# Optimization experiments

Measured on AMD Instinct MI355X. Metric: run time of the kernel, lower is better.

## Reference

```python
import jax, jax.numpy as jnp
import numpy as np

# Scalar quantization params (QLinear __init__ args)
FEATURE_BITWIDTH = 8
WEIGHT_BITWIDTH = 8
INPUT_ZERO_POINT = -3
OUTPUT_ZERO_POINT = -5
INPUT_SCALE = 0.05
OUTPUT_SCALE = 0.1
QMIN = -(1 << (FEATURE_BITWIDTH - 1))   # -128
QMAX = (1 << (FEATURE_BITWIDTH - 1)) - 1  # 127

M, K, N = 8192, 4096, 4096


def float_to_fixed_point(x, bitwidth):
    """Represent x (0 < x < 1) as int_scale * 2^-frac_bits with int_scale
    in [2^(bitwidth-2), 2^(bitwidth-1)) (mantissa fits in signed `bitwidth` bits)."""
    frac_bits = (bitwidth - 1 - jnp.ceil(jnp.log2(x))).astype(jnp.int32)
    int_scale = jnp.round(x * jnp.exp2(frac_bits.astype(jnp.float32))).astype(jnp.int32)
    return int_scale, frac_bits


def setup_inputs() -> dict:
    key = jax.random.key(0)
    k1, k2, k3, k4 = jax.random.split(key, 4)
    qinput = jax.random.randint(k1, (M, K), -128, 128, dtype=jnp.int8)
    qweight = jax.random.randint(k2, (N, K), -128, 128, dtype=jnp.int8)
    qbias = jax.random.randint(k3, (N,), -(1 << 16), 1 << 16, dtype=jnp.int32)
    # per-output-channel weight scale; keeps folded scale in (0, 1)
    weight_scale = jax.random.uniform(k4, (N,), jnp.float32, 0.002, 0.02)
    return {"qinput": qinput, "qweight": qweight, "qbias": qbias,
            "weight_scale": weight_scale}


def reference(qinput, qweight, qbias, weight_scale):
    w32 = qweight.astype(jnp.int32)                      # [N, K]
    # Qbias' = qbias - sum_k(qweight) * Zin  (bias shift folding input zero point)
    shifted_qbias = qbias - w32.sum(axis=1) * INPUT_ZERO_POINT  # [N]
    # int32 GEMM: [M, K] @ [K, N] + bias
    acc = qinput.astype(jnp.int32) @ w32.T + shifted_qbias[None, :]  # [M, N]
    # fixed-point requantization: (acc * int_scale) >> frac_bits + Zout
    folded_scale = INPUT_SCALE * weight_scale / OUTPUT_SCALE         # [N], in (0,1)
    int_scale, frac_bits = float_to_fixed_point(folded_scale, FEATURE_BITWIDTH)
    # widen to int64 for the multiply so the (acc * int_scale) product cannot wrap
    prod = acc.astype(jnp.int64) * int_scale.astype(jnp.int64)[None, :]
    scaled = jnp.right_shift(prod, frac_bits.astype(jnp.int64)[None, :])  # arithmetic >>
    out = scaled + OUTPUT_ZERO_POINT
    return jnp.clip(out, QMIN, QMAX).astype(jnp.int8)
```

## Files before the change

kernel.cpp:

```cpp
#include <hip/hip_runtime.h>
#include <cstdint>
#include <cstddef>

#define M_DIM 8192
#define N_DIM 4096
#define K_DIM 4096

#define BM 128
#define BN 128
#define BK 128

#define BM2 256
#define BN2 256
#define BK2 128
#define NKT (K_DIM / BK2)

typedef int int32x4  __attribute__((ext_vector_type(4)));
typedef int int32x16 __attribute__((ext_vector_type(16)));


typedef __attribute__((address_space(1))) const void* gas_cptr;
typedef __attribute__((address_space(3))) void* las_ptr;

__device__ __forceinline__ void async_copy16(const void* g, void* l) {
    __builtin_amdgcn_global_load_lds((gas_cptr)g, (las_ptr)l, 16, 0, 0);
}

__device__ __forceinline__ int32x4 pack16(const int* p) {
    const int32x4* v = (const int32x4*)p;
    int32x4 w0 = v[0], w1 = v[1], w2 = v[2], w3 = v[3];
    int32x4 r;
    r.x = (w0.x & 0xFF) | ((w0.y & 0xFF) << 8) | ((w0.z & 0xFF) << 16) | (w0.w << 24);
    r.y = (w1.x & 0xFF) | ((w1.y & 0xFF) << 8) | ((w1.z & 0xFF) << 16) | (w1.w << 24);
    r.z = (w2.x & 0xFF) | ((w2.y & 0xFF) << 8) | ((w2.z & 0xFF) << 16) | (w2.w << 24);
    r.w = (w3.x & 0xFF) | ((w3.y & 0xFF) << 8) | ((w3.z & 0xFF) << 16) | (w3.w << 24);
    return r;
}

__global__ void ql_detect_kernel(const int* a, const int* b, int* ws) {
    int t = threadIdx.x;
    int fa = 0, fb = 0;
    for (int i = t; i < 4096; i += 64) {
        int va = a[i]; if (va > 127 || va < -128) fa = 1;
        int vb = b[i]; if (vb > 127 || vb < -128) fb = 1;
    }
    unsigned long long ba = __ballot(fa);
    unsigned long long bb = __ballot(fb);
    if (t == 0) { ws[0] = ba ? 1 : 0; ws[1] = bb ? 1 : 0; }
}

#define PACK_WBLK 4096
#define PACK_ABLK 8192
__global__ __launch_bounds__(256)
void ql_pack2_kernel(const void* wsrc, int* wdst, const void* asrc, int* adst,
                     const int* qbias, const float* wscale, int* ws) {
    __shared__ int red[4];
    const int fA = __builtin_amdgcn_readfirstlane(ws[0]);
    const int fW = __builtin_amdgcn_readfirstlane(ws[1]);
    const int bid = blockIdx.x;
    const int tid = threadIdx.x;
    if (bid < PACK_WBLK) {
        if (fW) return;
        const int n = bid;
        const int32x4* src = (const int32x4*)wsrc + (size_t)n * 1024;
        int* dst = wdst + (size_t)n * 1024;
        int s = 0;
#pragma unroll
        for (int k = 0; k < 4; ++k) {
            const int i = k * 256 + tid;
            int32x4 v = src[i];
            s += v.x + v.y + v.z + v.w;
            dst[i] = (v.x & 0xFF) | ((v.y & 0xFF) << 8) | ((v.z & 0xFF) << 16) | (v.w << 24);
        }
#pragma unroll
        for (int off = 32; off > 0; off >>= 1) s += __shfl_down(s, off, 64);
        if ((tid & 63) == 0) red[tid >> 6] = s;
        __syncthreads();
        if (tid == 0) {
            const int st = red[0] + red[1] + red[2] + red[3];
            ws[16 + n] = qbias[n] + 3 * st;
            float folded = (0.05f * wscale[n]) / 0.1f;
            int fbits = (int)(7.0f - ceilf(log2f(folded)));
            int isc = (int)rintf(folded * exp2f((float)fbits));
            ws[16 + N_DIM + n] = isc;
            ws[16 + 2 * N_DIM + n] = fbits;
        }
    } else {
        if (fA) return;
        const long base = (long)(bid - PACK_WBLK) * 1024;
        const int32x4* src = (const int32x4*)asrc + base;
        int* dst = adst + base;
#pragma unroll
        for (int k = 0; k < 4; ++k) {
            const int i = k * 256 + tid;
            int32x4 v = src[i];
            dst[i] = (v.x & 0xFF) | ((v.y & 0xFF) << 8) | ((v.z & 0xFF) << 16) | (v.w << 24);
        }
    }
}

__global__ void ql_prep8_kernel(const void* worig, const int* qbias,
                                const float* wscale, int* ws) {
    const int fb = __builtin_amdgcn_readfirstlane(ws[1]);
    if (!fb) return;

    const int lane = threadIdx.x & 63;
    const int wid  = threadIdx.x >> 6;
    const int n = blockIdx.x * 4 + wid;

    const int32x4* row = (const int32x4*)((const int8_t*)worig + (size_t)n * K_DIM);
    int s = 0;
    for (int c = lane; c < K_DIM / 16; c += 64) {
        int32x4 v = row[c];
#pragma unroll
        for (int j = 0; j < 4; ++j) {
            int w = (j == 0) ? v.x : (j == 1) ? v.y : (j == 2) ? v.z : v.w;
            s += (int)(int8_t)(w) + (int)(int8_t)(w >> 8)
               + (int)(int8_t)(w >> 16) + (w >> 24);
        }
    }
#pragma unroll
    for (int off = 32; off > 0; off >>= 1) s += __shfl_down(s, off, 64);

    if (lane == 0) {
        ws[16 + n] = qbias[n] + 3 * s;
        float folded = (0.05f * wscale[n]) / 0.1f;
        int fbits = (int)(7.0f - ceilf(log2f(folded)));
        int isc = (int)rintf(folded * exp2f((float)fbits));
        ws[16 + N_DIM + n] = isc;
        ws[16 + 2 * N_DIM + n] = fbits;
    }
}

__global__ void ql_prep_kernel(const void* wptr, const int* qbias,
                               const float* wscale, int* ws) {
    const int lane = threadIdx.x & 63;
    const int wid  = threadIdx.x >> 6;
    const int n = blockIdx.x * 4 + wid;
    const int b8 = __builtin_amdgcn_readfirstlane(ws[1]);

    int s = 0;
    if (b8) {
        const int32x4* row = (const int32x4*)((const int8_t*)wptr + (size_t)n * K_DIM);
        for (int c = lane; c < K_DIM / 16; c += 64) {
            int32x4 v = row[c];
#pragma unroll
            for (int j = 0; j < 4; ++j) {
                int w = (j == 0) ? v.x : (j == 1) ? v.y : (j == 2) ? v.z : v.w;
                s += (int)(int8_t)(w) + (int)(int8_t)(w >> 8)
                   + (int)(int8_t)(w >> 16) + (w >> 24);
            }
        }
    } else {
        const int32x4* row = (const int32x4*)((const int*)wptr + (size_t)n * K_DIM);
        for (int c = lane; c < K_DIM / 4; c += 64) {
            int32x4 v = row[c];
            s += v.x + v.y + v.z + v.w;
        }
    }
#pragma unroll
    for (int off = 32; off > 0; off >>= 1) s += __shfl_down(s, off, 64);

    if (lane == 0) {
        ws[16 + n] = qbias[n] + 3 * s;
        float folded = (0.05f * wscale[n]) / 0.1f;
        int fbits = (int)(7.0f - ceilf(log2f(folded)));
        int isc = (int)rintf(folded * exp2f((float)fbits));
        ws[16 + N_DIM + n] = isc;
        ws[16 + 2 * N_DIM + n] = fbits;
    }
}

__device__ __forceinline__ void ql_epilogue(int32x4 acc[4][4], const int* ws,
                                            int* out, int bm, int bn,
                                            int wm, int wn, int qm, int qh) {
    const int* qb  = ws + 16;
    const int* isc = ws + 16 + N_DIM;
    const int* fbt = ws + 16 + 2 * N_DIM;
#pragma unroll
    for (int j = 0; j < 4; ++j) {
        const int n_g = bn * BN + wn + j * 16 + qm;
        const int b0 = qb[n_g];
        const int s0 = isc[n_g];
        const int f0 = fbt[n_g];
#pragma unroll
        for (int i = 0; i < 4; ++i) {
            const int m_base = bm * BM + wm + i * 16 + qh * 4;
#pragma unroll
            for (int r = 0; r < 4; ++r) {
                int v = ((r == 0) ? acc[i][j].x : (r == 1) ? acc[i][j].y
                        : (r == 2) ? acc[i][j].z : acc[i][j].w) + b0;
                long long p = (long long)v * (long long)s0;
                int o = (int)(p >> f0) - 5;
                o = o < -128 ? -128 : (o > 127 ? 127 : o);
                out[(size_t)(m_base + r) * N_DIM + n_g] = o;
            }
        }
    }
}


#define LOAD_AF(BUF, MH, DST) do { \
    _Pragma("unroll") for (int ml = 0; ml < 2; ++ml) \
    _Pragma("unroll") for (int kc = 0; kc < 4; ++kc) \
        DST[ml][kc] = LA[BUF][baseAe[kc] + (MH) * 512 + ml * 256]; \
} while (0)

#define LOAD_BF(BUF, NH, DST) do { \
    _Pragma("unroll") for (int kc = 0; kc < 4; ++kc) \
        DST[kc] = LB[BUF][baseBe[kc] + (NH) * 256]; \
} while (0)

#define MFMA_QUAD(MH, NH, AF, BF) do { \
    __builtin_amdgcn_s_setprio(1); \
    _Pragma("unroll") for (int kc = 0; kc < 4; ++kc) \
    _Pragma("unroll") for (int ml = 0; ml < 2; ++ml) \
        acc[(MH) * 2 + ml][NH] = __builtin_amdgcn_mfma_i32_32x32x32_i8( \
            AF[ml][kc], BF[kc], acc[(MH) * 2 + ml][NH], 0, 0, 0); \
    __builtin_amdgcn_s_setprio(0); \
} while (0)

#define STAGE_A(BUF, H, TT) do { \
    async_copy16(gA + (size_t)(TT) * 128 + (H) * 524288,          &LA[BUF][(H) * 1024 + t]); \
    async_copy16(gA + (size_t)(TT) * 128 + (H) * 524288 + 262144, &LA[BUF][(H) * 1024 + 512 + t]); \
} while (0)

#define STAGE_B(BUF, H, TT) do { \
    async_copy16(gB + (size_t)(TT) * 128 + (H) * 524288,          &LB[BUF][(H) * 1024 + t]); \
    async_copy16(gB + (size_t)(TT) * 128 + (H) * 524288 + 262144, &LB[BUF][(H) * 1024 + 512 + t]); \
} while (0)

#define TILE_BODY(BUF, TT, VMC) do { \
    asm volatile("s_waitcnt vmcnt(" #VMC ")" ::: "memory"); \
    __builtin_amdgcn_s_barrier(); \
    LOAD_AF(BUF, 0, afL); \
    LOAD_BF(BUF, 0, bf0); \
    if ((TT) + 1 < NKT) { STAGE_A(BUF ^ 1, 1, (TT) + 1); } \
    __builtin_amdgcn_s_barrier(); \
    MFMA_QUAD(0, 0, afL, bf0); \
    __builtin_amdgcn_s_barrier(); \
    LOAD_BF(BUF, 1, bf1); \
    if ((TT) + 1 < NKT) { STAGE_B(BUF ^ 1, 1, (TT) + 1); } \
    __builtin_amdgcn_s_barrier(); \
    MFMA_QUAD(0, 1, afL, bf1); \
    __builtin_amdgcn_s_barrier(); \
    LOAD_AF(BUF, 1, afH); \
    if ((TT) + 2 < NKT) { STAGE_B(BUF, 0, (TT) + 2); } \
    __builtin_amdgcn_s_barrier(); \
    MFMA_QUAD(1, 0, afH, bf0); \
    __builtin_amdgcn_s_barrier(); \
    if ((TT) + 2 < NKT) { STAGE_A(BUF, 0, (TT) + 2); } \
    __builtin_amdgcn_s_barrier(); \
    MFMA_QUAD(1, 1, afH, bf1); \
} while (0)

__global__ __launch_bounds__(512, 2)
void ql_gemm8_kernel(const void* a0, const int8_t* a8,
                     const void* b0, const int8_t* w8,
                     const int* ws, int* out) {
    __shared__ int32x4 LA[2][2048];
    __shared__ int32x4 LB[2][2048];

    const int fa = __builtin_amdgcn_readfirstlane(ws[0]);
    const int fb = __builtin_amdgcn_readfirstlane(ws[1]);
    const int8_t* aptr = fa ? (const int8_t*)a0 : a8;
    const int8_t* bptr = fb ? (const int8_t*)b0 : w8;

    const int t    = threadIdx.x;
    const int lane = t & 63;
    const int wid  = t >> 6;
    const int wr   = wid >> 2;
    const int wc   = wid & 3;
    const int l31  = lane & 31;
    const int hi   = lane >> 5;

    const int flat = blockIdx.y * gridDim.x + blockIdx.x;
    const int xcd  = flat & 7;
    const int lid  = flat >> 3;
    const int g    = lid >> 5;
    const int r    = lid & 31;
    const int bm   = xcd * 4 + g * 2 + (r & 1);
    const int bn   = r >> 1;

    const int arow0 = bm * BM2;
    const int brow0 = bn * BN2;

    const int fr = (lane & 7) ^ ((l31 >> 3) & 3);
    int baseAe[4], baseBe[4];
#pragma unroll
    for (int kc = 0; kc < 4; ++kc) {
        const int phys = (kc * 2 + hi) ^ fr;
        baseAe[kc] = (wr * 128 + l31) * 8 + phys;
        baseBe[kc] = (wc * 64  + l31) * 8 + phys;
    }

    const int colg = (t & 7) ^ ((t >> 3) & 7) ^ ((t >> 6) & 3);
    const int8_t* gA = aptr + (size_t)(arow0 + (t >> 3)) * K_DIM + colg * 16;
    const int8_t* gB = bptr + (size_t)(brow0 + (t >> 3)) * K_DIM + colg * 16;

    int32x16 acc[4][2] = {};
    int32x4 afL[2][4], afH[2][4], bf0[4], bf1[4];

    STAGE_A(0, 0, 0); STAGE_B(0, 0, 0);
    STAGE_A(0, 1, 0); STAGE_B(0, 1, 0);
    STAGE_B(1, 0, 1); STAGE_A(1, 0, 1);

#pragma unroll 1
    for (int T = 0; T < NKT - 2; T += 2) {
        TILE_BODY(0, T, 4);
        TILE_BODY(1, T + 1, 4);
    }
    TILE_BODY(0, NKT - 2, 4);
    TILE_BODY(1, NKT - 1, 0);

    const int* qb  = ws + 16;
    const int* isc = ws + 16 + N_DIM;
    const int* fbt = ws + 16 + 2 * N_DIM;
#pragma unroll
    for (int j = 0; j < 2; ++j) {
        const int n_g = bn * BN2 + wc * 64 + j * 32 + l31;
        const int b0r = qb[n_g];
        const int s0r = isc[n_g];
        const int f0r = fbt[n_g];
#pragma unroll
        for (int i = 0; i < 4; ++i) {
            const int m0 = bm * BM2 + wr * 128 + i * 32 + hi * 4;
#pragma unroll
            for (int reg = 0; reg < 16; ++reg) {
                const int row = (reg & 3) + 8 * (reg >> 2);
                int v = acc[i][j][reg] + b0r;
                long long p = (long long)v * (long long)s0r;
                int o = (int)(p >> f0r) - 5;
                o = o < -128 ? -128 : (o > 127 ? 127 : o);
                __builtin_nontemporal_store(o, &out[(size_t)(m0 + row) * N_DIM + n_g]);
            }
        }
    }
}

__global__ __launch_bounds__(256)
void ql_gemm_fb_kernel(const void* aptr, const void* bptr, const int* ws, int* out) {
    __shared__ int32x4 Als[BM * BK / 16];
    __shared__ int32x4 Bls[BN * BK / 16];

    const int a8 = __builtin_amdgcn_readfirstlane(ws[0]);
    const int b8 = __builtin_amdgcn_readfirstlane(ws[1]);

    const int t    = threadIdx.x;
    const int lane = t & 63;
    const int wid  = t >> 6;
    const int bn = blockIdx.x;
    const int bm = blockIdx.y;

    const int wm = (wid >> 1) * 64;
    const int wn = (wid & 1) * 64;
    const int qm = lane & 15;
    const int qh = lane >> 4;

    int32x4 acc[4][4] = {};

    for (int kt = 0; kt < K_DIM / BK; ++kt) {
        __syncthreads();
        const int k0 = kt * BK;
#pragma unroll
        for (int r = 0; r < 4; ++r) {
            const int c    = r * 256 + t;
            const int row  = c >> 3;
            const int colg = (c & 7) ^ (row & 7);
            const size_t offA = (size_t)(bm * BM + row) * K_DIM + k0 + colg * 16;
            const size_t offB = (size_t)(bn * BN + row) * K_DIM + k0 + colg * 16;
            if (a8) async_copy16((const int8_t*)aptr + offA, &Als[c]);
            else    Als[c] = pack16((const int*)aptr + offA);
            if (b8) async_copy16((const int8_t*)bptr + offB, &Bls[c]);
            else    Bls[c] = pack16((const int*)bptr + offB);
        }
        __syncthreads();

#pragma unroll
        for (int s = 0; s < 2; ++s) {
            const int colk = s * 4 + qh;
            int32x4 af[4], bf[4];
#pragma unroll
            for (int i = 0; i < 4; ++i) {
                const int ra = wm + i * 16 + qm;
                const int rb = wn + i * 16 + qm;
                af[i] = Als[ra * 8 + (colk ^ (ra & 7))];
                bf[i] = Bls[rb * 8 + (colk ^ (rb & 7))];
            }
#pragma unroll
            for (int i = 0; i < 4; ++i)
#pragma unroll
                for (int j = 0; j < 4; ++j)
                    acc[i][j] = __builtin_amdgcn_mfma_i32_16x16x64_i8(
                        af[i], bf[j], acc[i][j], 0, 0, 0);
        }
    }
    ql_epilogue(acc, ws, out, bm, bn, wm, wn, qm, qh);
}

extern "C" void kernel_launch(void* const* d_in, const int* in_sizes, int n_in,
                              void* d_out, int out_size, void* d_ws, size_t ws_size,
                              hipStream_t stream) {
    const void* qin    = d_in[0];
    const void* qwt    = d_in[1];
    const int* qbias   = (const int*)d_in[2];
    const float* wscal = (const float*)d_in[3];
    int* ws  = (int*)d_ws;
    int* out = (int*)d_out;

    hipLaunchKernelGGL(ql_detect_kernel, dim3(1), dim3(64), 0, stream,
                       (const int*)qin, (const int*)qwt, ws);

    const size_t need = 65536 + (size_t)M_DIM * K_DIM + (size_t)N_DIM * K_DIM;
    if (ws_size >= need) {
        int8_t* a8 = (int8_t*)d_ws + 65536;
        int8_t* w8 = a8 + (size_t)M_DIM * K_DIM;
        hipLaunchKernelGGL(ql_pack2_kernel, dim3(PACK_WBLK + PACK_ABLK), dim3(256),
                           0, stream, qwt, (int*)w8, qin, (int*)a8, qbias, wscal, ws);
        hipLaunchKernelGGL(ql_prep8_kernel, dim3(N_DIM / 4), dim3(256), 0, stream,
                           qwt, qbias, wscal, ws);
        hipLaunchKernelGGL(ql_gemm8_kernel, dim3(N_DIM / BN2, M_DIM / BM2), dim3(512),
                           0, stream, qin, a8, qwt, w8, ws, out);
    } else {
        hipLaunchKernelGGL(ql_prep_kernel, dim3(N_DIM / 4), dim3(256), 0, stream,
                           qwt, qbias, wscal, ws);
        hipLaunchKernelGGL(ql_gemm_fb_kernel, dim3(N_DIM / BN, M_DIM / BM), dim3(256), 0, stream,
                           qin, qwt, ws, out);
    }
}
```

Measured before the change: 416.0 us.

## Replace barrier-heavy interleaved pipeline with per-tile double buffering and staggered wave order

Replaces the fine-grained schedule, with eight barriers per K-tile and half-tile staging interleaved between MFMA quads, by a simple double buffer. Each tile issues all async copies for the next tile up front, computes the current tile, then ends with a single __syncthreads. Even and odd waves walk the four MFMA quads in opposite orders to spread LDS fragment reads across time. This cuts barrier overhead, but shrinks prefetch depth to one tile and leaves each tile waiting on all outstanding loads at its end, which risks exposing global-load latency.

```diff
diff --git a/kernel.cpp b/kernel.cpp
--- a/kernel.cpp
+++ b/kernel.cpp
@@ -220,38 +220,35 @@
     __builtin_amdgcn_s_setprio(0); \
 } while (0)
 
-#define STAGE_A(BUF, H, TT) do { \
-    async_copy16(gA + (size_t)(TT) * 128 + (H) * 524288,          &LA[BUF][(H) * 1024 + t]); \
-    async_copy16(gA + (size_t)(TT) * 128 + (H) * 524288 + 262144, &LA[BUF][(H) * 1024 + 512 + t]); \
+#define STAGE8(BUF, TT) do { \
+    _Pragma("unroll") for (int h2 = 0; h2 < 4; ++h2) { \
+        async_copy16(gA + (size_t)(TT) * 128 + (size_t)h2 * 262144, \
+                     &LA[BUF][h2 * 512 + t]); \
+        async_copy16(gB + (size_t)(TT) * 128 + (size_t)h2 * 262144, \
+                     &LB[BUF][h2 * 512 + t]); \
+    } \
 } while (0)
 
-#define STAGE_B(BUF, H, TT) do { \
-    async_copy16(gB + (size_t)(TT) * 128 + (H) * 524288,          &LB[BUF][(H) * 1024 + t]); \
-    async_copy16(gB + (size_t)(TT) * 128 + (H) * 524288 + 262144, &LB[BUF][(H) * 1024 + 512 + t]); \
-} while (0)
-
-#define TILE_BODY(BUF, TT, VMC) do { \
-    asm volatile("s_waitcnt vmcnt(" #VMC ")" ::: "memory"); \
-    __builtin_amdgcn_s_barrier(); \
-    LOAD_AF(BUF, 0, afL); \
-    LOAD_BF(BUF, 0, bf0); \
-    if ((TT) + 1 < NKT) { STAGE_A(BUF ^ 1, 1, (TT) + 1); } \
-    __builtin_amdgcn_s_barrier(); \
-    MFMA_QUAD(0, 0, afL, bf0); \
-    __builtin_amdgcn_s_barrier(); \
-    LOAD_BF(BUF, 1, bf1); \
-    if ((TT) + 1 < NKT) { STAGE_B(BUF ^ 1, 1, (TT) + 1); } \
-    __builtin_amdgcn_s_barrier(); \
-    MFMA_QUAD(0, 1, afL, bf1); \
-    __builtin_amdgcn_s_barrier(); \
-    LOAD_AF(BUF, 1, afH); \
-    if ((TT) + 2 < NKT) { STAGE_B(BUF, 0, (TT) + 2); } \
-    __builtin_amdgcn_s_barrier(); \
-    MFMA_QUAD(1, 0, afH, bf0); \
-    __builtin_amdgcn_s_barrier(); \
-    if ((TT) + 2 < NKT) { STAGE_A(BUF, 0, (TT) + 2); } \
-    __builtin_amdgcn_s_barrier(); \
-    MFMA_QUAD(1, 1, afH, bf1); \
+#define TILE2(BUF, TT) do { \
+    if (evenw) { LOAD_AF(BUF, 0, afL); LOAD_BF(BUF, 0, bf0); } \
+    else       { LOAD_AF(BUF, 1, afH); LOAD_BF(BUF, 1, bf1); } \
+    if ((TT) + 1 < NKT) { STAGE8((BUF) ^ 1, (TT) + 1); } \
+    if (evenw) { \
+        MFMA_QUAD(0, 0, afL, bf0); \
+        LOAD_BF(BUF, 1, bf1); \
+        MFMA_QUAD(0, 1, afL, bf1); \
+        LOAD_AF(BUF, 1, afH); \
+        MFMA_QUAD(1, 0, afH, bf0); \
+        MFMA_QUAD(1, 1, afH, bf1); \
+    } else { \
+        MFMA_QUAD(1, 1, afH, bf1); \
+        LOAD_BF(BUF, 0, bf0); \
+        MFMA_QUAD(1, 0, afH, bf0); \
+        LOAD_AF(BUF, 0, afL); \
+        MFMA_QUAD(0, 0, afL, bf0); \
+        MFMA_QUAD(0, 1, afL, bf1); \
+    } \
+    __syncthreads(); \
 } while (0)
 
 __global__ __launch_bounds__(512, 2)
@@ -273,6 +270,7 @@
     const int wc   = wid & 3;
     const int l31  = lane & 31;
     const int hi   = lane >> 5;
+    const bool evenw = (wid & 1) == 0;
 
     const int flat = blockIdx.y * gridDim.x + blockIdx.x;
     const int xcd  = flat & 7;
@@ -301,17 +299,14 @@
     int32x16 acc[4][2] = {};
     int32x4 afL[2][4], afH[2][4], bf0[4], bf1[4];
 
-    STAGE_A(0, 0, 0); STAGE_B(0, 0, 0);
-    STAGE_A(0, 1, 0); STAGE_B(0, 1, 0);
-    STAGE_B(1, 0, 1); STAGE_A(1, 0, 1);
+    STAGE8(0, 0);
+    __syncthreads();
 
 #pragma unroll 1
-    for (int T = 0; T < NKT - 2; T += 2) {
-        TILE_BODY(0, T, 4);
-        TILE_BODY(1, T + 1, 4);
-    }
-    TILE_BODY(0, NKT - 2, 4);
-    TILE_BODY(1, NKT - 1, 0);
+    for (int T = 0; T < NKT; T += 2) {
+        TILE2(0, T);
+        TILE2(1, T + 1);
+    }
 
     const int* qb  = ws + 16;
     const int* isc = ws + 16 + N_DIM;
```

Result: no change. 415.2 us (-0.2%).
